# Kernel optimization log

Measured on AMD Instinct MI355X. Metric: run time of the kernel, lower is better.

The kernel has to match this reference:

```python
import jax, jax.numpy as jnp
import numpy as np

B, S, D = 1, 1024, 64
_EPS = 1e-15
_BND = 1.0 - 1e-7  # artanh domain clamp (mirrors geoopt projection)


def _sq(x):
    return jnp.sum(x * x, axis=-1, keepdims=True)


def _nrm(x):
    return jnp.sqrt(_sq(x) + _EPS)


def _normalize(x, axis, eps):
    n = jnp.sqrt(jnp.sum(x * x, axis=axis, keepdims=True))
    return x / jnp.maximum(n, eps)


def _mobius_add(x, y):
    x2, y2 = _sq(x), _sq(y)
    xy = jnp.sum(x * y, axis=-1, keepdims=True)
    num = (1.0 + 2.0 * xy + y2) * x + (1.0 - x2) * y
    den = 1.0 + 2.0 * xy + x2 * y2
    return num / jnp.maximum(den, _EPS)


def _expmap0(u):
    n = _nrm(u)
    return jnp.tanh(n) * u / n


def _logmap0(y):
    n = _nrm(y)
    return jnp.arctanh(jnp.clip(n, 0.0, _BND)) * y / n


def _dist(x, y):
    n = _nrm(_mobius_add(-x, y))[..., 0]
    return 2.0 * jnp.arctanh(jnp.clip(n, 0.0, _BND))


def _logmap(x, y):
    d = _mobius_add(-x, y)
    n = _nrm(d)
    lam = 2.0 / jnp.maximum(1.0 - _sq(x), _EPS)
    return (2.0 / lam) * jnp.arctanh(jnp.clip(n, 0.0, _BND)) * d / n


def _transp0back(x, v):
    return v / jnp.maximum(1.0 - _sq(x), _EPS)


def _forward(q_in, k_in, v_in, Wq, bq, Wk, bk, Wv, bv, Wo, bo,
             tau, gamma, tangent_scale, gumbel_u, v_rand_init):
    q = q_in @ Wq.T + bq
    k = k_in @ Wk.T + bk
    v = v_in @ Wv.T + bv

    q_hyp = _expmap0(q)   # [B,S,D]
    k_hyp = _expmap0(k)

    # all-pairs geodesic distances [B,S,S]
    dist = _dist(q_hyp[:, :, None, :], k_hyp[:, None, :, :])
    min_d = jnp.min(dist, axis=-1, keepdims=True)
    w_un = jnp.exp(-(dist - min_d))                         # unnormalized weights
    w_sum = jnp.sum(w_un, axis=-1, keepdims=True) + 1e-8
    w_probs = w_un / w_sum
    h = jnp.einsum('bqk,bkd->bqd', w_probs, v)

    # Einstein midpoint: weighted Euclidean centroid of pre-map keys -> manifold
    centroid_euc = jnp.einsum('bqk,bkd->bqd', w_un / w_sum, k)
    centroid_hyp = _expmap0(centroid_euc)                   # [B,S,D]

    c2k = _dist(centroid_hyp[:, :, None, :], k_hyp[:, None, :, :])  # [B,S,S]
    wnv = w_un / w_sum
    entropy = -jnp.sum(wnv * jnp.log(wnv + 1e-8), axis=-1, keepdims=True)
    eff_mass = jnp.exp(entropy)
    variance = jnp.sum(wnv * c2k ** 2, axis=-1, keepdims=True)
    tension = variance - tau * eff_mass                     # [B,S,1]

    # matrix-free TPCA power iteration on weighted local tangents
    k_local = _logmap(centroid_hyp[:, :, None, :], k_hyp[:, None, :, :])  # [B,S,S,D]
    weighted_k = k_local * jnp.sqrt(w_un[..., None] + 1e-8)
    v_r = _normalize(v_rand_init, axis=2, eps=1e-12)        # [B,S,D,1]
    for _ in range(3):
        proj = jnp.einsum('bqkd,bqdo->bqko', weighted_k, v_r)
        v_r = jnp.einsum('bqkd,bqko->bqdo', weighted_k, proj)
        v_r = _normalize(v_r, axis=2, eps=1e-12)
    w_proj_local = v_r[..., 0]                              # [B,S,D]
    w_proj_global = _transp0back(centroid_hyp, w_proj_local)

    q_tan = _logmap0(q_hyp)
    c_tan = _logmap0(centroid_hyp)
    fallback = _normalize(q_tan - c_tan, axis=-1, eps=1e-8)
    w_proj = jnp.where(variance > 1e-5, w_proj_global, fallback)

    h_norm = _nrm(h)
    h_comp = jnp.arcsinh(h_norm) * (h / (h_norm + 1e-8))

    # Pitchfork bifurcation (c = 1)
    x = jnp.sum(h_comp * w_proj, axis=-1, keepdims=True)
    diss = (tension > 0).astype(h.dtype)
    h_mag = _nrm(h_comp)
    amplitude = h_mag * jnp.tanh(tension) * diss
    g = -jnp.log(-jnp.log(gumbel_u))                        # gumbel noise, logits = 0
    y_soft = jax.nn.softmax(g / 0.5, axis=-1)
    y_hard = jax.nn.one_hot(jnp.argmax(y_soft, axis=-1), 2, dtype=h.dtype)
    gp = y_soft + jax.lax.stop_gradient(y_hard - y_soft)    # straight-through
    eps_g = (gp[..., 0] - gp[..., 1])[..., None]            # gp @ [1,-1]
    x_star = eps_g * amplitude
    delta_c = jnp.tanh(x_star - x)
    h_prime = h_comp + delta_c * w_proj
    hp_norm = _nrm(h_prime) + 1e-8
    h_pb = h_prime * (jnp.tanh(hp_norm * tangent_scale) / hp_norm)
    h_prime_hyp = _expmap0(h_pb)

    h_out_bif = _logmap0(h_prime_hyp)
    gate = jax.nn.sigmoid(gamma)
    h_fused = (1.0 - gate) * h + gate * h_out_bif
    return h_fused @ Wo.T + bo


def setup_inputs() -> dict:
    key = jax.random.key(0)
    ks = jax.random.split(key, 10)
    std = 0.02
    return {
        'q_in': jax.random.normal(ks[0], (B, S, D), jnp.float32),
        'k_in': jax.random.normal(ks[1], (B, S, D), jnp.float32),
        'v_in': jax.random.normal(ks[2], (B, S, D), jnp.float32),
        'Wq': std * jax.random.normal(ks[3], (D, D), jnp.float32),
        'bq': jnp.zeros((D,), jnp.float32),
        'Wk': std * jax.random.normal(ks[4], (D, D), jnp.float32),
        'bk': jnp.zeros((D,), jnp.float32),
        'Wv': std * jax.random.normal(ks[5], (D, D), jnp.float32),
        'bv': jnp.zeros((D,), jnp.float32),
        'Wo': std * jax.random.normal(ks[6], (D, D), jnp.float32),
        'bo': jnp.zeros((D,), jnp.float32),
        'tau': jnp.float32(5.0),
        'gamma': jnp.float32(0.0),
        'tangent_scale': jnp.float32(0.1),
        'gumbel_u': jax.random.uniform(ks[7], (B, S, 2), jnp.float32, 1e-6, 1.0 - 1e-6),
        'v_rand_init': jax.random.normal(ks[8], (B, S, D, 1), jnp.float32),
    }


def reference(q_in, k_in, v_in, Wq, bq, Wk, bk, Wv, bv, Wo, bo,
              tau, gamma, tangent_scale, gumbel_u, v_rand_init):
    return _forward(q_in, k_in, v_in, Wq, bq, Wk, bk, Wv, bv, Wo, bo,
                    tau, gamma, tangent_scale, gumbel_u, v_rand_init)
```

## Files before the change

kernel.cpp:

```cpp
#include <hip/hip_runtime.h>
#include <math.h>

#define S 1024
#define D 64
#define BND 0.99999994f
#define FINF 3.4e38f
#define C4(v,c) ((&(v).x)[c])

__device__ __forceinline__ float waveSum(float v){
  #pragma unroll
  for(int o=32;o>0;o>>=1) v += __shfl_xor(v,o,64);
  return v;
}
__device__ __forceinline__ float4 mk4(const float* a){
  float4 r; r.x=a[0]; r.y=a[1]; r.z=a[2]; r.w=a[3]; return r;
}
__device__ __forceinline__ float4 blockSum512_v4(float4 v, float4* red4){
  #pragma unroll
  for(int o=32;o>0;o>>=1){
    v.x+=__shfl_xor(v.x,o,64); v.y+=__shfl_xor(v.y,o,64);
    v.z+=__shfl_xor(v.z,o,64); v.w+=__shfl_xor(v.w,o,64);
  }
  const int wid=threadIdx.x>>6;
  __syncthreads();
  if((threadIdx.x&63)==0) red4[wid]=v;
  __syncthreads();
  float4 s={0.f,0.f,0.f,0.f};
  #pragma unroll
  for(int k=0;k<8;k++){ float4 r=red4[k]; s.x+=r.x; s.y+=r.y; s.z+=r.z; s.w+=r.w; }
  return s;
}
__device__ __forceinline__ float4 blockMin512_v4(float4 v, float4* red4){
  #pragma unroll
  for(int o=32;o>0;o>>=1){
    v.x=fminf(v.x,__shfl_xor(v.x,o,64)); v.y=fminf(v.y,__shfl_xor(v.y,o,64));
    v.z=fminf(v.z,__shfl_xor(v.z,o,64)); v.w=fminf(v.w,__shfl_xor(v.w,o,64));
  }
  const int wid=threadIdx.x>>6;
  __syncthreads();
  if((threadIdx.x&63)==0) red4[wid]=v;
  __syncthreads();
  float4 s=red4[0];
  #pragma unroll
  for(int k=1;k<8;k++){ float4 r=red4[k]; s.x=fminf(s.x,r.x); s.y=fminf(s.y,r.y); s.z=fminf(s.z,r.z); s.w=fminf(s.w,r.w); }
  return s;
}

__global__ __launch_bounds__(64) void k_proj(
  const float* __restrict__ qin, const float* __restrict__ kin, const float* __restrict__ vin,
  const float* __restrict__ Wq, const float* __restrict__ bq,
  const float* __restrict__ Wk, const float* __restrict__ bk,
  const float* __restrict__ Wv, const float* __restrict__ bv,
  const float* __restrict__ vrand,
  float* __restrict__ q_hyp, float* __restrict__ k_hyp, float* __restrict__ kT,
  float* __restrict__ vproj, float* __restrict__ kproj,
  float* __restrict__ q2, float* __restrict__ k2, float* __restrict__ v_r)
{
  const int i = blockIdx.x, d = threadIdx.x;
  __shared__ __align__(16) float lq[D], lk[D], lv[D];
  lq[d]=qin[i*D+d]; lk[d]=kin[i*D+d]; lv[d]=vin[i*D+d];
  __syncthreads();
  float aq=bq[d], ak=bk[d], av=bv[d];
  const float4* wq4=(const float4*)(Wq + d*D);
  const float4* wk4=(const float4*)(Wk + d*D);
  const float4* wv4=(const float4*)(Wv + d*D);
  #pragma unroll
  for(int e=0;e<16;e++){
    float4 a=wq4[e], b=wk4[e], c=wv4[e];
    aq += lq[4*e]*a.x + lq[4*e+1]*a.y + lq[4*e+2]*a.z + lq[4*e+3]*a.w;
    ak += lk[4*e]*b.x + lk[4*e+1]*b.y + lk[4*e+2]*b.z + lk[4*e+3]*b.w;
    av += lv[4*e]*c.x + lv[4*e+1]*c.y + lv[4*e+2]*c.z + lv[4*e+3]*c.w;
  }
  float nq = sqrtf(waveSum(aq*aq)+1e-15f);
  float qh = tanhf(nq)*aq/nq;
  q_hyp[i*D+d]=qh;
  float q2v = waveSum(qh*qh);
  if(d==0) q2[i]=q2v;
  float nk = sqrtf(waveSum(ak*ak)+1e-15f);
  float kh = tanhf(nk)*ak/nk;
  k_hyp[i*D+d]=kh;
  kT[(size_t)d*S + i]=kh;
  float k2v = waveSum(kh*kh);
  if(d==0) k2[i]=k2v;
  vproj[i*D+d]=av;
  kproj[i*D+d]=ak;
  float vr = vrand[i*D+d];
  float nn = sqrtf(waveSum(vr*vr));
  v_r[i*D+d] = vr/fmaxf(nn,1e-12f);
}

__global__ __launch_bounds__(512,2) void k_fused(
  const float* __restrict__ q_hyp_g, const float* __restrict__ k_hyp,
  const float* __restrict__ kT,
  const float* __restrict__ q2a, const float* __restrict__ k2a,
  const float* __restrict__ vproj, const float* __restrict__ kproj,
  const float* __restrict__ v_r, const float* __restrict__ tau_p,
  const float* __restrict__ gu, const float* __restrict__ gamma_p,
  const float* __restrict__ ts_p, const float* __restrict__ Wo,
  const float* __restrict__ bo, float* __restrict__ out)
{
  const int i0=blockIdx.x*4, tid=threadIdx.x;
  __shared__ __align__(16) float qv[4][D];
  __shared__ __align__(16) float cv[4][D];
  __shared__ __align__(16) float vv[4][D];
  __shared__ __align__(16) float hl[4][D];
  __shared__ __align__(16) float fus[4][D];
  __shared__ __align__(16) float wl[4][S];
  __shared__ __align__(16) float aal[4][S];
  __shared__ __align__(16) float bbl[4][S];
  __shared__ __align__(16) float4 sA[2048];
  __shared__ __align__(16) float4 red4[8];
  __shared__ float scal[4][6];
  float* const pA=(float*)sA;

  if(tid<256){ qv[tid>>6][tid&63]=q_hyp_g[i0*D+tid]; vv[tid>>6][tid&63]=v_r[i0*D+tid]; }
  __syncthreads();

  const int jf=tid&255, dh=tid>>8;
  const int qq0=dh, qq1=dh+2;
  const int dq=tid&15, g=tid>>4;
  const float4* kT4=(const float4*)kT;
  const float tau=tau_p[0];

  {
    float4 p0={0,0,0,0},p1={0,0,0,0},p2={0,0,0,0},p3={0,0,0,0};
    #pragma unroll 8
    for(int dd=0; dd<32; ++dd){
      const int d=(dh<<5)+dd;
      const float4 y=kT4[d*256+jf];
      const float c0=qv[0][d], c1=qv[1][d], c2q=qv[2][d], c3=qv[3][d];
      p0.x+=c0*y.x; p0.y+=c0*y.y; p0.z+=c0*y.z; p0.w+=c0*y.w;
      p1.x+=c1*y.x; p1.y+=c1*y.y; p1.z+=c1*y.z; p1.w+=c1*y.w;
      p2.x+=c2q*y.x; p2.y+=c2q*y.y; p2.z+=c2q*y.z; p2.w+=c2q*y.w;
      p3.x+=c3*y.x; p3.y+=c3*y.y; p3.z+=c3*y.z; p3.w+=c3*y.w;
    }
    sA[(dh*4+0)*256+jf]=p0; sA[(dh*4+1)*256+jf]=p1;
    sA[(dh*4+2)*256+jf]=p2; sA[(dh*4+3)*256+jf]=p3;
  }
  __syncthreads();
  float4 inv4;
  {
    const float4 y2v=((const float4*)k2a)[jf];
    const float x2q[2]={q2a[i0+qq0], q2a[i0+qq1]};
    float dist[2][4];
    float4 mn4={FINF,FINF,FINF,FINF};
    #pragma unroll
    for(int it=0; it<2; ++it){
      const int qq = it? qq1:qq0;
      const float4 da=sA[(0*4+qq)*256+jf], db=sA[(1*4+qq)*256+jf];
      const float x2=x2q[it], B=1.f-x2;
      #pragma unroll
      for(int c=0;c<4;c++){
        const float y2=C4(y2v,c);
        const float dot=C4(da,c)+C4(db,c);
        const float A=1.f-2.f*dot+y2;
        const float den=fmaxf(1.f-2.f*dot+x2*y2,1e-15f);
        const float num2=fmaxf(A*A*x2 + B*B*y2 - 2.f*A*B*dot, 0.f);
        const float nn=sqrtf(num2/(den*den)+1e-15f);
        dist[it][c]=2.f*atanhf(fminf(nn,BND));
        C4(mn4,qq)=fminf(C4(mn4,qq),dist[it][c]);
      }
    }
    mn4=blockMin512_v4(mn4,red4);
    float w[2][4];
    float4 s4={0,0,0,0};
    #pragma unroll
    for(int it=0; it<2; ++it){
      const int qq = it? qq1:qq0;
      #pragma unroll
      for(int c=0;c<4;c++){ w[it][c]=expf(C4(mn4,qq)-dist[it][c]); C4(s4,qq)+=w[it][c]; }
      ((float4*)&wl[qq][0])[jf]=mk4(w[it]);
    }
    s4=blockSum512_v4(s4,red4);
    inv4.x=1.f/(s4.x+1e-8f); inv4.y=1.f/(s4.y+1e-8f);
    inv4.z=1.f/(s4.z+1e-8f); inv4.w=1.f/(s4.w+1e-8f);
    float4 e4={0,0,0,0};
    #pragma unroll
    for(int it=0; it<2; ++it){
      const int qq = it? qq1:qq0;
      #pragma unroll
      for(int c=0;c<4;c++){
        const float p=w[it][c]*C4(inv4,qq);
        C4(e4,qq) -= p*logf(p+1e-8f);
      }
    }
    e4=blockSum512_v4(e4,red4);
    if(tid<4) scal[tid][3]=expf(C4(e4,tid));
  }

  {
    float4 a0={0,0,0,0},a1={0,0,0,0},a2={0,0,0,0},a3={0,0,0,0};
    #pragma unroll 4
    for(int jj=0;jj<32;jj++){
      const int j=jj*32+g;
      const float4 y=((const float4*)(vproj + j*D))[dq];
      const float u0=wl[0][j],u1=wl[1][j],u2=wl[2][j],u3=wl[3][j];
      a0.x+=u0*y.x; a0.y+=u0*y.y; a0.z+=u0*y.z; a0.w+=u0*y.w;
      a1.x+=u1*y.x; a1.y+=u1*y.y; a1.z+=u1*y.z; a1.w+=u1*y.w;
      a2.x+=u2*y.x; a2.y+=u2*y.y; a2.z+=u2*y.z; a2.w+=u2*y.w;
      a3.x+=u3*y.x; a3.y+=u3*y.y; a3.z+=u3*y.z; a3.w+=u3*y.w;
    }
    __syncthreads();
    *(float4*)&pA[(g*4+0)*64+dq*4]=a0; *(float4*)&pA[(g*4+1)*64+dq*4]=a1;
    *(float4*)&pA[(g*4+2)*64+dq*4]=a2; *(float4*)&pA[(g*4+3)*64+dq*4]=a3;
    __syncthreads();
    if(tid<256){
      const int q=tid>>6, d=tid&63;
      float hs=0.f;
      #pragma unroll 8
      for(int gg=0;gg<32;gg++) hs+=pA[(gg*4+q)*64+d];
      hl[q][d]=hs*C4(inv4,q);
    }
    __syncthreads();
    float4 b0={0,0,0,0},b1={0,0,0,0},b2={0,0,0,0},b3={0,0,0,0};
    #pragma unroll 4
    for(int jj=0;jj<32;jj++){
      const int j=jj*32+g;
      const float4 y=((const float4*)(kproj + j*D))[dq];
      const float u0=wl[0][j],u1=wl[1][j],u2=wl[2][j],u3=wl[3][j];
      b0.x+=u0*y.x; b0.y+=u0*y.y; b0.z+=u0*y.z; b0.w+=u0*y.w;
      b1.x+=u1*y.x; b1.y+=u1*y.y; b1.z+=u1*y.z; b1.w+=u1*y.w;
      b2.x+=u2*y.x; b2.y+=u2*y.y; b2.z+=u2*y.z; b2.w+=u2*y.w;
      b3.x+=u3*y.x; b3.y+=u3*y.y; b3.z+=u3*y.z; b3.w+=u3*y.w;
    }
    *(float4*)&pA[(g*4+0)*64+dq*4]=b0; *(float4*)&pA[(g*4+1)*64+dq*4]=b1;
    *(float4*)&pA[(g*4+2)*64+dq*4]=b2; *(float4*)&pA[(g*4+3)*64+dq*4]=b3;
    __syncthreads();
    if(tid<256){
      const int q=tid>>6, d=tid&63;
      float cs=0.f;
      #pragma unroll 8
      for(int gg=0;gg<32;gg++) cs+=pA[(gg*4+q)*64+d];
      const float ca=cs*C4(inv4,q);
      const float n=sqrtf(waveSum(ca*ca)+1e-15f);
      const float ch=tanhf(n)*ca/n;
      cv[q][d]=ch;
      const float c2v=waveSum(ch*ch);
      if(d==0) scal[q][4]=c2v;
    }
  }
  __syncthreads();

  {
    float4 p0={0,0,0,0},p1={0,0,0,0},p2={0,0,0,0},p3={0,0,0,0};
    #pragma unroll 8
    for(int dd=0; dd<32; ++dd){
      const int d=(dh<<5)+dd;
      const float4 y=kT4[d*256+jf];
      const float c0=cv[0][d], c1=cv[1][d], c2q=cv[2][d], c3=cv[3][d];
      p0.x+=c0*y.x; p0.y+=c0*y.y; p0.z+=c0*y.z; p0.w+=c0*y.w;
      p1.x+=c1*y.x; p1.y+=c1*y.y; p1.z+=c1*y.z; p1.w+=c1*y.w;
      p2.x+=c2q*y.x; p2.y+=c2q*y.y; p2.z+=c2q*y.z; p2.w+=c2q*y.w;
      p3.x+=c3*y.x; p3.y+=c3*y.y; p3.z+=c3*y.z; p3.w+=c3*y.w;
    }
    sA[(dh*4+0)*256+jf]=p0; sA[(dh*4+1)*256+jf]=p1;
    sA[(dh*4+2)*256+jf]=p2; sA[(dh*4+3)*256+jf]=p3;
  }
  __syncthreads();
  {
    const float4 y2v=((const float4*)k2a)[jf];
    float4 var4={0,0,0,0};
    #pragma unroll
    for(int it=0; it<2; ++it){
      const int qq = it? qq1:qq0;
      const float4 da=sA[(0*4+qq)*256+jf], db=sA[(1*4+qq)*256+jf];
      const float4 wv=((float4*)&wl[qq][0])[jf];
      const float x2=scal[qq][4];
      const float Bc=1.f-x2, mB=fmaxf(Bc,1e-15f), inv=C4(inv4,qq);
      float ac[4], bc[4];
      #pragma unroll
      for(int c=0;c<4;c++){
        const float y2=C4(y2v,c);
        const float dot=C4(da,c)+C4(db,c);
        const float A=1.f-2.f*dot+y2;
        const float den=fmaxf(1.f-2.f*dot+x2*y2,1e-15f);
        const float num2=fmaxf(A*A*x2+Bc*Bc*y2-2.f*A*Bc*dot,0.f);
        const float nn=sqrtf(num2/(den*den)+1e-15f);
        const float art=atanhf(fminf(nn,BND));
        const float w=C4(wv,c);
        C4(var4,qq) += w*inv*4.f*art*art;
        const float coef=sqrtf(w+1e-8f)*mB*art/(nn*den);
        ac[c]=-coef*A; bc[c]=coef*Bc;
      }
      ((float4*)&aal[qq][0])[jf]=mk4(ac);
      ((float4*)&bbl[qq][0])[jf]=mk4(bc);
    }
    var4=blockSum512_v4(var4,red4);
    if(tid<4){ scal[tid][0]=C4(var4,tid); scal[tid][1]=C4(var4,tid) - tau*scal[tid][3]; }
  }
  float* const prow0=&wl[0][0];

  for(int it3=0; it3<3; ++it3){
    __syncthreads();
    if(tid<256){
      const int q=tid>>6, d=tid&63;
      const float cd=waveSum(cv[q][d]*vv[q][d]);
      if(d==0) scal[q][2]=cd;
    }
    __syncthreads();
    const float cd0=scal[0][2], cd1=scal[1][2], cd2=scal[2][2], cd3=scal[3][2];
    {
      float4 p0={0,0,0,0},p1={0,0,0,0},p2={0,0,0,0},p3={0,0,0,0};
      #pragma unroll 8
      for(int dd=0; dd<32; ++dd){
        const int d=(dh<<5)+dd;
        const float4 y=kT4[d*256+jf];
        const float c0=vv[0][d], c1=vv[1][d], c2q=vv[2][d], c3=vv[3][d];
        p0.x+=c0*y.x; p0.y+=c0*y.y; p0.z+=c0*y.z; p0.w+=c0*y.w;
        p1.x+=c1*y.x; p1.y+=c1*y.y; p1.z+=c1*y.z; p1.w+=c1*y.w;
        p2.x+=c2q*y.x; p2.y+=c2q*y.y; p2.z+=c2q*y.z; p2.w+=c2q*y.w;
        p3.x+=c3*y.x; p3.y+=c3*y.y; p3.z+=c3*y.z; p3.w+=c3*y.w;
      }
      sA[(dh*4+0)*256+jf]=p0; sA[(dh*4+1)*256+jf]=p1;
      sA[(dh*4+2)*256+jf]=p2; sA[(dh*4+3)*256+jf]=p3;
    }
    __syncthreads();
    float4 sal4={0,0,0,0};
    {
      const float cdq[2]={ dh? cd1:cd0, dh? cd3:cd2 };
      #pragma unroll
      for(int it=0; it<2; ++it){
        const int qq = it? qq1:qq0;
        const float4 da=sA[(0*4+qq)*256+jf], db=sA[(1*4+qq)*256+jf];
        const float4 av=((float4*)&aal[qq][0])[jf];
        const float4 bv=((float4*)&bbl[qq][0])[jf];
        float pr[4];
        #pragma unroll
        for(int c=0;c<4;c++){
          const float t=C4(da,c)+C4(db,c);
          const float p=C4(av,c)*cdq[it] + C4(bv,c)*t;
          pr[c]=p*C4(bv,c);
          C4(sal4,qq) += p*C4(av,c);
        }
        ((float4*)&prow0[qq*S])[jf]=mk4(pr);
      }
    }
    sal4=blockSum512_v4(sal4,red4);
    {
      float4 a0={0,0,0,0},a1={0,0,0,0},a2={0,0,0,0},a3={0,0,0,0};
      #pragma unroll 4
      for(int jj=0;jj<32;jj++){
        const int j=jj*32+g;
        const float4 y=((const float4*)(k_hyp + j*D))[dq];
        const float u0=prow0[0*S+j],u1=prow0[1*S+j],u2=prow0[2*S+j],u3=prow0[3*S+j];
        a0.x+=u0*y.x; a0.y+=u0*y.y; a0.z+=u0*y.z; a0.w+=u0*y.w;
        a1.x+=u1*y.x; a1.y+=u1*y.y; a1.z+=u1*y.z; a1.w+=u1*y.w;
        a2.x+=u2*y.x; a2.y+=u2*y.y; a2.z+=u2*y.z; a2.w+=u2*y.w;
        a3.x+=u3*y.x; a3.y+=u3*y.y; a3.z+=u3*y.z; a3.w+=u3*y.w;
      }
      *(float4*)&pA[(g*4+0)*64+dq*4]=a0; *(float4*)&pA[(g*4+1)*64+dq*4]=a1;
      *(float4*)&pA[(g*4+2)*64+dq*4]=a2; *(float4*)&pA[(g*4+3)*64+dq*4]=a3;
    }
    __syncthreads();
    if(tid<256){
      const int q=tid>>6, d=tid&63;
      float od=C4(sal4,q)*cv[q][d];
      #pragma unroll 8
      for(int gg=0;gg<32;gg++) od += pA[(gg*4+q)*64+d];
      const float nn=sqrtf(waveSum(od*od));
      vv[q][d]=od/fmaxf(nn,1e-12f);
    }
  }
  __syncthreads();

  if(tid<256){
    const int q=tid>>6, d=tid&63;
    const int i=i0+q;
    const float x2q_c=scal[q][4];
    const float vd=vv[q][d];
    const float vars=scal[q][0], tns=scal[q][1];
    const float hd=hl[q][d];
    const float qd=qv[q][d];
    const float q2=q2a[i];
    const float wpg=vd/fmaxf(1.f-x2q_c,1e-15f);
    const float nq=sqrtf(q2+1e-15f);
    const float qt=atanhf(fminf(nq,BND))*qd/nq;
    const float ncn=sqrtf(x2q_c+1e-15f);
    const float ct=atanhf(fminf(ncn,BND))*cv[q][d]/ncn;
    const float df=qt-ct;
    const float nd=sqrtf(waveSum(df*df));
    const float fb=df/fmaxf(nd,1e-8f);
    const float wp=(vars>1e-5f)?wpg:fb;
    const float hn=sqrtf(waveSum(hd*hd)+1e-15f);
    const float hc=asinhf(hn)*hd/(hn+1e-8f);
    const float x=waveSum(hc*wp);
    const float hmag=sqrtf(waveSum(hc*hc)+1e-15f);
    const float amp=(tns>0.f)? hmag*tanhf(tns) : 0.f;
    const float u0=gu[i*2], u1=gu[i*2+1];
    const float eg=(u0>=u1)?1.f:-1.f;
    const float dc=tanhf(eg*amp - x);
    const float hp=hc+dc*wp;
    const float hpn=sqrtf(waveSum(hp*hp)+1e-15f)+1e-8f;
    const float hpb=hp*(tanhf(hpn*ts_p[0])/hpn);
    const float n2=sqrtf(waveSum(hpb*hpb)+1e-15f);
    const float hyp=tanhf(n2)*hpb/n2;
    const float n3=sqrtf(waveSum(hyp*hyp)+1e-15f);
    const float bif=atanhf(fminf(n3,BND))*hyp/n3;
    const float gate=1.f/(1.f+expf(-gamma_p[0]));
    fus[q][d]=(1.f-gate)*hd + gate*bif;
  }
  __syncthreads();
  if(tid<256){
    const int q=tid>>6, d=tid&63;
    float acc=bo[d];
    const float4* wo4=(const float4*)(Wo + d*D);
    #pragma unroll
    for(int e=0;e<16;e++){
      float4 wv=wo4[e];
      acc += fus[q][4*e]*wv.x + fus[q][4*e+1]*wv.y + fus[q][4*e+2]*wv.z + fus[q][4*e+3]*wv.w;
    }
    out[(i0+q)*D+d]=acc;
  }
}

extern "C" void kernel_launch(void* const* d_in, const int* in_sizes, int n_in,
                              void* d_out, int out_size, void* d_ws, size_t ws_size,
                              hipStream_t stream)
{
  const float* qin=(const float*)d_in[0];
  const float* kin=(const float*)d_in[1];
  const float* vin=(const float*)d_in[2];
  const float* Wq=(const float*)d_in[3];
  const float* bq=(const float*)d_in[4];
  const float* Wk=(const float*)d_in[5];
  const float* bk=(const float*)d_in[6];
  const float* Wv=(const float*)d_in[7];
  const float* bv=(const float*)d_in[8];
  const float* Wo=(const float*)d_in[9];
  const float* bo=(const float*)d_in[10];
  const float* tau=(const float*)d_in[11];
  const float* gamma=(const float*)d_in[12];
  const float* tscale=(const float*)d_in[13];
  const float* gu=(const float*)d_in[14];
  const float* vrand=(const float*)d_in[15];
  float* out=(float*)d_out;

  float* p=(float*)d_ws;
  float* q_hyp=p; p+=S*D;
  float* k_hyp=p; p+=S*D;
  float* kT=p;    p+=S*D;
  float* vproj=p; p+=S*D;
  float* kproj=p; p+=S*D;
  float* v_r=p;   p+=S*D;
  float* q2=p;   p+=S;
  float* k2=p;   p+=S;

  k_proj<<<S,64,0,stream>>>(qin,kin,vin,Wq,bq,Wk,bk,Wv,bv,vrand,
                            q_hyp,k_hyp,kT,vproj,kproj,q2,k2,v_r);
  k_fused<<<S/4,512,0,stream>>>(q_hyp,k_hyp,kT,q2,k2,vproj,kproj,v_r,
                                tau,gu,gamma,tscale,Wo,bo,out);
}
```

Before: 89.96 us.

## Keep kT slice in registers across passes and transpose small vectors for float4 LDS

Loads each thread's 32 float4 slice of the transposed key matrix into registers once and reuses it for the q, centroid and three iterative v projections, instead of re-reading it from global memory each pass. The q/c/v vectors are stored transposed so one float4 shared-memory read yields all four query coefficients. The c·v dot product is folded into the previous normalization step, removing a sync and a reduction per iteration. The 128 extra VGPRs under launch_bounds(512,2) risk spills or lower occupancy.

```diff
diff --git a/kernel.cpp b/kernel.cpp
--- a/kernel.cpp
+++ b/kernel.cpp
@@ -6,6 +6,7 @@
 #define BND 0.99999994f
 #define FINF 3.4e38f
 #define C4(v,c) ((&(v).x)[c])
+#define FMA4(acc,s,v) { (acc).x+=(s)*(v).x; (acc).y+=(s)*(v).y; (acc).z+=(s)*(v).z; (acc).w+=(s)*(v).w; }
 
 __device__ __forceinline__ float waveSum(float v){
   #pragma unroll
@@ -100,9 +101,9 @@
   const float* __restrict__ bo, float* __restrict__ out)
 {
   const int i0=blockIdx.x*4, tid=threadIdx.x;
-  __shared__ __align__(16) float qv[4][D];
-  __shared__ __align__(16) float cv[4][D];
-  __shared__ __align__(16) float vv[4][D];
+  __shared__ __align__(16) float qvT[D*4];
+  __shared__ __align__(16) float cvT[D*4];
+  __shared__ __align__(16) float vvT[D*4];
   __shared__ __align__(16) float hl[4][D];
   __shared__ __align__(16) float fus[4][D];
   __shared__ __align__(16) float wl[4][S];
@@ -113,26 +114,30 @@
   __shared__ float scal[4][6];
   float* const pA=(float*)sA;
 
-  if(tid<256){ qv[tid>>6][tid&63]=q_hyp_g[i0*D+tid]; vv[tid>>6][tid&63]=v_r[i0*D+tid]; }
-  __syncthreads();
-
   const int jf=tid&255, dh=tid>>8;
   const int qq0=dh, qq1=dh+2;
   const int dq=tid&15, g=tid>>4;
+  const float tau=tau_p[0];
   const float4* kT4=(const float4*)kT;
-  const float tau=tau_p[0];
+
+  float4 Y[32];
+  #pragma unroll
+  for(int dd=0;dd<32;dd++) Y[dd]=kT4[(dh*32+dd)*256+jf];
+
+  if(tid<256){
+    const int q=tid>>6, d=tid&63;
+    qvT[d*4+q]=q_hyp_g[(i0+q)*D+d];
+    vvT[d*4+q]=v_r[(i0+q)*D+d];
+  }
+  __syncthreads();
 
   {
     float4 p0={0,0,0,0},p1={0,0,0,0},p2={0,0,0,0},p3={0,0,0,0};
-    #pragma unroll 8
-    for(int dd=0; dd<32; ++dd){
-      const int d=(dh<<5)+dd;
-      const float4 y=kT4[d*256+jf];
-      const float c0=qv[0][d], c1=qv[1][d], c2q=qv[2][d], c3=qv[3][d];
-      p0.x+=c0*y.x; p0.y+=c0*y.y; p0.z+=c0*y.z; p0.w+=c0*y.w;
-      p1.x+=c1*y.x; p1.y+=c1*y.y; p1.z+=c1*y.z; p1.w+=c1*y.w;
-      p2.x+=c2q*y.x; p2.y+=c2q*y.y; p2.z+=c2q*y.z; p2.w+=c2q*y.w;
-      p3.x+=c3*y.x; p3.y+=c3*y.y; p3.z+=c3*y.z; p3.w+=c3*y.w;
+    #pragma unroll
+    for(int dd=0;dd<32;dd++){
+      const float4 qd=*(const float4*)&qvT[(dh*32+dd)*4];
+      FMA4(p0,qd.x,Y[dd]); FMA4(p1,qd.y,Y[dd]);
+      FMA4(p2,qd.z,Y[dd]); FMA4(p3,qd.w,Y[dd]);
     }
     sA[(dh*4+0)*256+jf]=p0; sA[(dh*4+1)*256+jf]=p1;
     sA[(dh*4+2)*256+jf]=p2; sA[(dh*4+3)*256+jf]=p3;
@@ -195,10 +200,7 @@
       const int j=jj*32+g;
       const float4 y=((const float4*)(vproj + j*D))[dq];
       const float u0=wl[0][j],u1=wl[1][j],u2=wl[2][j],u3=wl[3][j];
-      a0.x+=u0*y.x; a0.y+=u0*y.y; a0.z+=u0*y.z; a0.w+=u0*y.w;
-      a1.x+=u1*y.x; a1.y+=u1*y.y; a1.z+=u1*y.z; a1.w+=u1*y.w;
-      a2.x+=u2*y.x; a2.y+=u2*y.y; a2.z+=u2*y.z; a2.w+=u2*y.w;
-      a3.x+=u3*y.x; a3.y+=u3*y.y; a3.z+=u3*y.z; a3.w+=u3*y.w;
+      FMA4(a0,u0,y); FMA4(a1,u1,y); FMA4(a2,u2,y); FMA4(a3,u3,y);
     }
     __syncthreads();
     *(float4*)&pA[(g*4+0)*64+dq*4]=a0; *(float4*)&pA[(g*4+1)*64+dq*4]=a1;
@@ -218,10 +220,7 @@
       const int j=jj*32+g;
       const float4 y=((const float4*)(kproj + j*D))[dq];
       const float u0=wl[0][j],u1=wl[1][j],u2=wl[2][j],u3=wl[3][j];
-      b0.x+=u0*y.x; b0.y+=u0*y.y; b0.z+=u0*y.z; b0.w+=u0*y.w;
-      b1.x+=u1*y.x; b1.y+=u1*y.y; b1.z+=u1*y.z; b1.w+=u1*y.w;
-      b2.x+=u2*y.x; b2.y+=u2*y.y; b2.z+=u2*y.z; b2.w+=u2*y.w;
-      b3.x+=u3*y.x; b3.y+=u3*y.y; b3.z+=u3*y.z; b3.w+=u3*y.w;
+      FMA4(b0,u0,y); FMA4(b1,u1,y); FMA4(b2,u2,y); FMA4(b3,u3,y);
     }
     *(float4*)&pA[(g*4+0)*64+dq*4]=b0; *(float4*)&pA[(g*4+1)*64+dq*4]=b1;
     *(float4*)&pA[(g*4+2)*64+dq*4]=b2; *(float4*)&pA[(g*4+3)*64+dq*4]=b3;
@@ -234,24 +233,21 @@
       const float ca=cs*C4(inv4,q);
       const float n=sqrtf(waveSum(ca*ca)+1e-15f);
       const float ch=tanhf(n)*ca/n;
-      cv[q][d]=ch;
+      cvT[d*4+q]=ch;
       const float c2v=waveSum(ch*ch);
-      if(d==0) scal[q][4]=c2v;
+      const float cd=waveSum(ch*vvT[d*4+q]);
+      if(d==0){ scal[q][4]=c2v; scal[q][2]=cd; }
     }
   }
   __syncthreads();
 
   {
     float4 p0={0,0,0,0},p1={0,0,0,0},p2={0,0,0,0},p3={0,0,0,0};
-    #pragma unroll 8
-    for(int dd=0; dd<32; ++dd){
-      const int d=(dh<<5)+dd;
-      const float4 y=kT4[d*256+jf];
-      const float c0=cv[0][d], c1=cv[1][d], c2q=cv[2][d], c3=cv[3][d];
-      p0.x+=c0*y.x; p0.y+=c0*y.y; p0.z+=c0*y.z; p0.w+=c0*y.w;
-      p1.x+=c1*y.x; p1.y+=c1*y.y; p1.z+=c1*y.z; p1.w+=c1*y.w;
-      p2.x+=c2q*y.x; p2.y+=c2q*y.y; p2.z+=c2q*y.z; p2.w+=c2q*y.w;
-      p3.x+=c3*y.x; p3.y+=c3*y.y; p3.z+=c3*y.z; p3.w+=c3*y.w;
+    #pragma unroll
+    for(int dd=0;dd<32;dd++){
+      const float4 cd4=*(const float4*)&cvT[(dh*32+dd)*4];
+      FMA4(p0,cd4.x,Y[dd]); FMA4(p1,cd4.y,Y[dd]);
+      FMA4(p2,cd4.z,Y[dd]); FMA4(p3,cd4.w,Y[dd]);
     }
     sA[(dh*4+0)*256+jf]=p0; sA[(dh*4+1)*256+jf]=p1;
     sA[(dh*4+2)*256+jf]=p2; sA[(dh*4+3)*256+jf]=p3;
@@ -292,24 +288,13 @@
 
   for(int it3=0; it3<3; ++it3){
     __syncthreads();
-    if(tid<256){
-      const int q=tid>>6, d=tid&63;
-      const float cd=waveSum(cv[q][d]*vv[q][d]);
-      if(d==0) scal[q][2]=cd;
-    }
-    __syncthreads();
-    const float cd0=scal[0][2], cd1=scal[1][2], cd2=scal[2][2], cd3=scal[3][2];
     {
       float4 p0={0,0,0,0},p1={0,0,0,0},p2={0,0,0,0},p3={0,0,0,0};
-      #pragma unroll 8
-      for(int dd=0; dd<32; ++dd){
-        const int d=(dh<<5)+dd;
-        const float4 y=kT4[d*256+jf];
-        const float c0=vv[0][d], c1=vv[1][d], c2q=vv[2][d], c3=vv[3][d];
-        p0.x+=c0*y.x; p0.y+=c0*y.y; p0.z+=c0*y.z; p0.w+=c0*y.w;
-        p1.x+=c1*y.x; p1.y+=c1*y.y; p1.z+=c1*y.z; p1.w+=c1*y.w;
-        p2.x+=c2q*y.x; p2.y+=c2q*y.y; p2.z+=c2q*y.z; p2.w+=c2q*y.w;
-        p3.x+=c3*y.x; p3.y+=c3*y.y; p3.z+=c3*y.z; p3.w+=c3*y.w;
+      #pragma unroll
+      for(int dd=0;dd<32;dd++){
+        const float4 vd4=*(const float4*)&vvT[(dh*32+dd)*4];
+        FMA4(p0,vd4.x,Y[dd]); FMA4(p1,vd4.y,Y[dd]);
+        FMA4(p2,vd4.z,Y[dd]); FMA4(p3,vd4.w,Y[dd]);
       }
       sA[(dh*4+0)*256+jf]=p0; sA[(dh*4+1)*256+jf]=p1;
       sA[(dh*4+2)*256+jf]=p2; sA[(dh*4+3)*256+jf]=p3;
@@ -317,7 +302,7 @@
     __syncthreads();
     float4 sal4={0,0,0,0};
     {
-      const float cdq[2]={ dh? cd1:cd0, dh? cd3:cd2 };
+      const float cdq[2]={scal[qq0][2], scal[qq1][2]};
       #pragma unroll
       for(int it=0; it<2; ++it){
         const int qq = it? qq1:qq0;
@@ -343,10 +328,7 @@
         const int j=jj*32+g;
         const float4 y=((const float4*)(k_hyp + j*D))[dq];
         const float u0=prow0[0*S+j],u1=prow0[1*S+j],u2=prow0[2*S+j],u3=prow0[3*S+j];
-        a0.x+=u0*y.x; a0.y+=u0*y.y; a0.z+=u0*y.z; a0.w+=u0*y.w;
-        a1.x+=u1*y.x; a1.y+=u1*y.y; a1.z+=u1*y.z; a1.w+=u1*y.w;
-        a2.x+=u2*y.x; a2.y+=u2*y.y; a2.z+=u2*y.z; a2.w+=u2*y.w;
-        a3.x+=u3*y.x; a3.y+=u3*y.y; a3.z+=u3*y.z; a3.w+=u3*y.w;
+        FMA4(a0,u0,y); FMA4(a1,u1,y); FMA4(a2,u2,y); FMA4(a3,u3,y);
       }
       *(float4*)&pA[(g*4+0)*64+dq*4]=a0; *(float4*)&pA[(g*4+1)*64+dq*4]=a1;
       *(float4*)&pA[(g*4+2)*64+dq*4]=a2; *(float4*)&pA[(g*4+3)*64+dq*4]=a3;
@@ -354,11 +336,14 @@
     __syncthreads();
     if(tid<256){
       const int q=tid>>6, d=tid&63;
-      float od=C4(sal4,q)*cv[q][d];
+      float od=C4(sal4,q)*cvT[d*4+q];
       #pragma unroll 8
       for(int gg=0;gg<32;gg++) od += pA[(gg*4+q)*64+d];
       const float nn=sqrtf(waveSum(od*od));
-      vv[q][d]=od/fmaxf(nn,1e-12f);
+      const float vn=od/fmaxf(nn,1e-12f);
+      vvT[d*4+q]=vn;
+      const float cd=waveSum(cvT[d*4+q]*vn);
+      if(d==0) scal[q][2]=cd;
     }
   }
   __syncthreads();
@@ -367,16 +352,16 @@
     const int q=tid>>6, d=tid&63;
     const int i=i0+q;
     const float x2q_c=scal[q][4];
-    const float vd=vv[q][d];
+    const float vd=vvT[d*4+q];
     const float vars=scal[q][0], tns=scal[q][1];
     const float hd=hl[q][d];
-    const float qd=qv[q][d];
+    const float qd=qvT[d*4+q];
     const float q2=q2a[i];
     const float wpg=vd/fmaxf(1.f-x2q_c,1e-15f);
     const float nq=sqrtf(q2+1e-15f);
     const float qt=atanhf(fminf(nq,BND))*qd/nq;
     const float ncn=sqrtf(x2q_c+1e-15f);
-    const float ct=atanhf(fminf(ncn,BND))*cv[q][d]/ncn;
+    const float ct=atanhf(fminf(ncn,BND))*cvT[d*4+q]/ncn;
     const float df=qt-ct;
     const float nd=sqrtf(waveSum(df*df));
     const float fb=df/fmaxf(nd,1e-8f);
```

After: 86.81 us. 3.5% less time.
